# Kernel tuning notes

Hardware: AMD Instinct MI355X
Metric: run time of the kernel (lower is better)

The kernel has to match this reference:

```python
import jax, jax.numpy as jnp
import numpy as np

N = 50000
E = 800000
IN_DIM = 128
H1 = 512
H2 = 300
OUT_DIM = 10
EPS = 1e-5


def setup_inputs() -> dict:
    key = jax.random.key(0)
    ks = jax.random.split(key, 12)
    x = jax.random.normal(ks[0], (N, IN_DIM), dtype=jnp.float32)
    edge_index = jax.random.randint(ks[1], (2, E), 0, N, dtype=jnp.int64)
    edge_weight = jax.random.uniform(ks[2], (E,), dtype=jnp.float32)
    def glorot(k, fan_in, fan_out):
        lim = np.sqrt(6.0 / (fan_in + fan_out)).astype(np.float32)
        return jax.random.uniform(k, (fan_in, fan_out), jnp.float32, -lim, lim)
    return {
        "x": x,
        "edge_index": edge_index,
        "edge_weight": edge_weight,
        "W1": glorot(ks[3], IN_DIM, H1), "b1": jnp.zeros((H1,), jnp.float32),
        "g1": jnp.ones((H1,), jnp.float32), "beta1": jnp.zeros((H1,), jnp.float32),
        "W2": glorot(ks[4], H1, H2), "b2": jnp.zeros((H2,), jnp.float32),
        "g2": jnp.ones((H2,), jnp.float32), "beta2": jnp.zeros((H2,), jnp.float32),
        "Wl": glorot(ks[5], H2, OUT_DIM), "bl": jnp.zeros((OUT_DIM,), jnp.float32),
    }


def _gcn_norm(edge_index, edge_weight, n):
    # add self loops (fill value 1.0), then symmetric normalization (PyG gcn_norm)
    si = jnp.arange(n, dtype=edge_index.dtype)
    row = jnp.concatenate([edge_index[0], si])  # source
    col = jnp.concatenate([edge_index[1], si])  # target
    w = jnp.concatenate([edge_weight, jnp.ones((n,), edge_weight.dtype)])
    deg = jax.ops.segment_sum(w, col, num_segments=n)
    dis = jnp.where(deg > 0, jax.lax.rsqrt(deg), 0.0)
    return row, col, dis[row] * w * dis[col]


def _propagate(h, row, col, norm, n):
    # gather source rows, weight, scatter-add into targets
    return jax.ops.segment_sum(h[row] * norm[:, None], col, num_segments=n)


def _batchnorm(h, g, beta):
    mean = jnp.mean(h, axis=0)
    var = jnp.mean(jnp.square(h - mean), axis=0)  # biased var (torch BN)
    return (h - mean) * jax.lax.rsqrt(var + EPS) * g + beta


def reference(x, edge_index, edge_weight, W1, b1, g1, beta1,
              W2, b2, g2, beta2, Wl, bl):
    n = x.shape[0]
    row, col, norm = _gcn_norm(edge_index, edge_weight, n)
    # layer 1: aggregate then transform (== GCNConv's lin-then-propagate math)
    h = _propagate(x, row, col, norm, n) @ W1 + b1
    h = jax.nn.relu(_batchnorm(h, g1, beta1))
    # layer 2: transform then aggregate
    h = _propagate(h @ W2, row, col, norm, n) + b2
    h = jax.nn.relu(_batchnorm(h, g2, beta2))
    # classifier head + log_softmax
    h = jax.nn.relu(h @ Wl + bl)
    return jax.nn.log_softmax(h, axis=1)
```

## Files before the change

### kernel.cpp

```cpp
#include <hip/hip_runtime.h>
#include <math.h>

namespace {

constexpr int kIn  = 128;
constexpr int kH1  = 512;
constexpr int kH2  = 300;
constexpr int kH2p = 304;
constexpr int kW2R = 384;
constexpr int kOut = 10;
constexpr float kEps = 1e-5f;

typedef __attribute__((ext_vector_type(8))) short bf16x8;
typedef __attribute__((ext_vector_type(4))) float f32x4;

__device__ __forceinline__ void atomAddF(float* p, float v) { unsafeAtomicAdd(p, v); }

__device__ __forceinline__ unsigned short f2bf(float f) {
  unsigned u = __builtin_bit_cast(unsigned, f);
  unsigned r = u + 0x7fffu + ((u >> 16) & 1u);
  return (unsigned short)(r >> 16);
}
__device__ __forceinline__ float bf2f(unsigned short h) {
  return __builtin_bit_cast(float, (unsigned)h << 16);
}
__device__ __forceinline__ float blo(unsigned u) { return __builtin_bit_cast(float, u << 16); }
__device__ __forceinline__ float bhi(unsigned u) { return __builtin_bit_cast(float, u & 0xffff0000u); }
__device__ __forceinline__ unsigned pk2(float a, float b) {
  return (unsigned)f2bf(a) | ((unsigned)f2bf(b) << 16);
}

__device__ __forceinline__ void gload16(const unsigned short* g, unsigned short* l) {
  __builtin_amdgcn_global_load_lds(
      (const __attribute__((address_space(1))) unsigned int*)g,
      (__attribute__((address_space(3))) unsigned int*)l, 16, 0, 0);
}

__device__ __forceinline__ void fma8(const uint4& q, float w, float* acc) {
  acc[0] = fmaf(blo(q.x), w, acc[0]);
  acc[1] = fmaf(bhi(q.x), w, acc[1]);
  acc[2] = fmaf(blo(q.y), w, acc[2]);
  acc[3] = fmaf(bhi(q.y), w, acc[3]);
  acc[4] = fmaf(blo(q.z), w, acc[4]);
  acc[5] = fmaf(bhi(q.z), w, acc[5]);
  acc[6] = fmaf(blo(q.w), w, acc[6]);
  acc[7] = fmaf(bhi(q.w), w, acc[7]);
}

__global__ void k_prep(float* __restrict__ deg, int* __restrict__ cnt,
                       const float* __restrict__ x, unsigned short* __restrict__ xbf,
                       float* __restrict__ st,
                       const float* __restrict__ W1, unsigned short* __restrict__ W1T,
                       const float* __restrict__ W2, unsigned short* __restrict__ W2T, int n) {
  int i = blockIdx.x * blockDim.x + threadIdx.x;
  if (i < n) { deg[i] = 1.0f; cnt[i] = 0; }
  if (i < 4096) st[i] = 0.f;
  if (i < kIn * kH1) {
    int nn = i / kIn, k = i - nn * kIn;
    W1T[i] = f2bf(W1[(size_t)k * kH1 + nn]);
  }
  if (i < kW2R * kH1) {
    int nn = i / kH1, k = i - nn * kH1;
    W2T[i] = (nn < kH2) ? f2bf(W2[(size_t)k * kH2 + nn]) : (unsigned short)0;
  }
  if (i < n * 16) {
    int node = i >> 4, g = i & 15;
    const float4* xp = reinterpret_cast<const float4*>(x + (size_t)node * kIn + g * 8);
    float4 v0 = xp[0], v1 = xp[1];
    uint4 o;
    o.x = pk2(v0.x, v0.y); o.y = pk2(v0.z, v0.w);
    o.z = pk2(v1.x, v1.y); o.w = pk2(v1.z, v1.w);
    reinterpret_cast<uint4*>(xbf)[i] = o;
  }
}

__global__ void k_deg_cnt(float* __restrict__ deg, int* __restrict__ cnt,
                          const int* __restrict__ ei, const float* __restrict__ w, int nE) {
  int i = blockIdx.x * blockDim.x + threadIdx.x;
  if (i < nE) {
    int c = ei[nE + i];
    atomAddF(&deg[c], w[i]);
    atomicAdd(&cnt[c], 1);
  }
}

__global__ void k_dis(float* __restrict__ deg, int n) {
  int i = blockIdx.x * blockDim.x + threadIdx.x;
  if (i < n) deg[i] = rsqrtf(deg[i]);
}

__global__ __launch_bounds__(1024) void k_scan(int* __restrict__ cnt, int n) {
  __shared__ int wsum[16];
  __shared__ int woff[17];
  const int lane = threadIdx.x & 63;
  const int wid  = threadIdx.x >> 6;
  int carry = 0;
  const int nchunk = (n + 1023) >> 10;
  for (int ch = 0; ch < nchunk; ++ch) {
    int i = (ch << 10) + threadIdx.x;
    int v = (i < n) ? cnt[i] : 0;
    int s = v;
#pragma unroll
    for (int off = 1; off < 64; off <<= 1) {
      int t = __shfl_up(s, off);
      if (lane >= off) s += t;
    }
    if (lane == 63) wsum[wid] = s;
    __syncthreads();
    if (wid == 0 && lane < 16) {
      int u = wsum[lane];
#pragma unroll
      for (int off = 1; off < 16; off <<= 1) {
        int q = __shfl_up(u, off);
        if (lane >= off) u += q;
      }
      woff[lane + 1] = u;
      if (lane == 0) woff[0] = 0;
    }
    __syncthreads();
    int excl = s - v + woff[wid] + carry;
    if (i < n) cnt[i] = excl;
    carry += woff[16];
    __syncthreads();
  }
}

__global__ void k_scatter(int* __restrict__ cnt, const int* __restrict__ ei,
                          const float* __restrict__ w, const float* __restrict__ dis,
                          uint2* __restrict__ pr, int nE) {
  int i = blockIdx.x * blockDim.x + threadIdx.x;
  if (i < nE) {
    int r = ei[i];
    int c = ei[nE + i];
    int pos = atomicAdd(&cnt[c], 1);
    float ww = dis[r] * w[i] * dis[c];
    pr[pos] = make_uint2((unsigned)r, __builtin_bit_cast(unsigned, ww));
  }
}

template<int NSQ>
__global__ void k_gather(const unsigned short* __restrict__ X, const int* __restrict__ endp,
                         const uint2* __restrict__ pr, const float* __restrict__ dis,
                         unsigned short* __restrict__ out, int n) {
  int tid = blockIdx.x * blockDim.x + threadIdx.x;
  int v = tid / NSQ;
  int s = tid - v * NSQ;
  if (v >= n) return;
  int beg = (v == 0) ? 0 : endp[v - 1];
  int end = endp[v];
  const uint4* Xr = reinterpret_cast<const uint4*>(X);
  float d = dis[v];
  float sw = d * d;
  float acc[8];
  {
    uint4 q = Xr[(size_t)v * NSQ + s];
    acc[0] = blo(q.x) * sw; acc[1] = bhi(q.x) * sw;
    acc[2] = blo(q.y) * sw; acc[3] = bhi(q.y) * sw;
    acc[4] = blo(q.z) * sw; acc[5] = bhi(q.z) * sw;
    acc[6] = blo(q.w) * sw; acc[7] = bhi(q.w) * sw;
  }
  int e = beg;
  for (; e + 4 <= end; e += 4) {
    uint2 p0 = pr[e], p1 = pr[e + 1], p2 = pr[e + 2], p3 = pr[e + 3];
    uint4 q0 = Xr[(size_t)p0.x * NSQ + s];
    uint4 q1 = Xr[(size_t)p1.x * NSQ + s];
    uint4 q2 = Xr[(size_t)p2.x * NSQ + s];
    uint4 q3 = Xr[(size_t)p3.x * NSQ + s];
    fma8(q0, __builtin_bit_cast(float, p0.y), acc);
    fma8(q1, __builtin_bit_cast(float, p1.y), acc);
    fma8(q2, __builtin_bit_cast(float, p2.y), acc);
    fma8(q3, __builtin_bit_cast(float, p3.y), acc);
  }
  for (; e < end; ++e) {
    uint2 p = pr[e];
    uint4 q = Xr[(size_t)p.x * NSQ + s];
    fma8(q, __builtin_bit_cast(float, p.y), acc);
  }
  uint4 o;
  o.x = pk2(acc[0], acc[1]);
  o.y = pk2(acc[2], acc[3]);
  o.z = pk2(acc[4], acc[5]);
  o.w = pk2(acc[6], acc[7]);
  reinterpret_cast<uint4*>(out)[(size_t)v * NSQ + s] = o;
}

__global__ __launch_bounds__(256) void k_gemm(const unsigned short* __restrict__ A,
    const unsigned short* __restrict__ BT, unsigned short* __restrict__ C,
    int M, int Nlog, int K, int ntiles, int nwg) {
  constexpr int BK = 64;
  __shared__ unsigned short lA[(BK / 8) * 128 * 8];
  __shared__ unsigned short lB[(BK / 8) * 128 * 8];

  int p = blockIdx.x;
  int xcd = p & 7, idx = p >> 3;
  int q8 = nwg >> 3, r8 = nwg & 7;
  int logical = (xcd < r8 ? xcd * (q8 + 1) : r8 * (q8 + 1) + (xcd - r8) * q8) + idx;
  const int nt = logical % ntiles;
  const int mt = logical / ntiles;
  const int m0 = mt * 128, n0 = nt * 128;

  const int tid = threadIdx.x, lane = tid & 63, wid = tid >> 6;
  const int wr = wid >> 1, wc = wid & 1;
  const int fr = lane & 15, fq = lane >> 4;

  int arow[4], brow[4], k8s[4];
#pragma unroll
  for (int j = 0; j < 4; ++j) {
    int g = tid + 256 * j;
    int row = g & 127;
    k8s[j] = g >> 7;
    int ar = m0 + row;
    arow[j] = (ar < M) ? ar : (M - 1);
    brow[j] = n0 + row;
  }

  f32x4 acc[4][4] = {};

  for (int k0 = 0; k0 < K; k0 += BK) {
    __syncthreads();
#pragma unroll
    for (int j = 0; j < 4; ++j) {
      int g = tid + 256 * j;
      gload16(A  + (size_t)arow[j] * K + k0 + k8s[j] * 8, &lA[g * 8]);
      gload16(BT + (size_t)brow[j] * K + k0 + k8s[j] * 8, &lB[g * 8]);
    }
    __syncthreads();
#pragma unroll
    for (int step = 0; step < 2; ++step) {
      bf16x8 af[4], bf[4];
#pragma unroll
      for (int m = 0; m < 4; ++m)
        af[m] = *reinterpret_cast<const bf16x8*>(
            &lA[(((step * 4 + fq) << 7) + wr * 64 + m * 16 + fr) * 8]);
#pragma unroll
      for (int nn = 0; nn < 4; ++nn)
        bf[nn] = *reinterpret_cast<const bf16x8*>(
            &lB[(((step * 4 + fq) << 7) + wc * 64 + nn * 16 + fr) * 8]);
#pragma unroll
      for (int m = 0; m < 4; ++m)
#pragma unroll
        for (int nn = 0; nn < 4; ++nn)
          acc[m][nn] = __builtin_amdgcn_mfma_f32_16x16x32_bf16(af[m], bf[nn], acc[m][nn], 0, 0, 0);
    }
  }

#pragma unroll
  for (int m = 0; m < 4; ++m) {
#pragma unroll
    for (int r = 0; r < 4; ++r) {
      int row = m0 + wr * 64 + m * 16 + fq * 4 + r;
      if (row >= M) continue;
#pragma unroll
      for (int nn = 0; nn < 4; ++nn) {
        int col = n0 + wc * 64 + nn * 16 + fr;
        if (col < Nlog)
          C[(size_t)row * Nlog + col] = f2bf(acc[m][nn][r]);
      }
    }
  }
}

__global__ void k_bn_stats_bf16(const unsigned short* __restrict__ H, float* __restrict__ s1,
                                float* __restrict__ s2, int n, int C, int stride, int rpb) {
  int r0 = blockIdx.x * rpb;
  int r1 = r0 + rpb;
  if (r1 > n) r1 = n;
  for (int c = threadIdx.x; c < C; c += blockDim.x) {
    float a = 0.f, b = 0.f;
    for (int r = r0; r < r1; ++r) {
      float v = bf2f(H[(size_t)r * stride + c]);
      a += v;
      b = fmaf(v, v, b);
    }
    atomAddF(&s1[c], a);
    atomAddF(&s2[c], b);
  }
}

__global__ void k_bn_finalize(const float* __restrict__ s1, const float* __restrict__ s2,
                              const float* __restrict__ g, const float* __restrict__ beta,
                              float* __restrict__ scale, float* __restrict__ shift,
                              int C, float invN) {
  int c = blockIdx.x * blockDim.x + threadIdx.x;
  if (c >= C) return;
  float mean = s1[c] * invN;
  float var = fmaxf(s2[c] * invN - mean * mean, 0.f);
  float sc = g[c] * rsqrtf(var + kEps);
  scale[c] = sc;
  shift[c] = beta[c] - mean * sc;
}

template<int C>
__global__ void k_bn_apply_relu_bf16(unsigned short* __restrict__ H,
                                     const float* __restrict__ scale,
                                     const float* __restrict__ shift, int total8) {
  int i = blockIdx.x * blockDim.x + threadIdx.x;
  if (i >= total8) return;
  uint4 q = reinterpret_cast<uint4*>(H)[i];
  int c = (i * 8) & (C - 1);
  unsigned w[4] = {q.x, q.y, q.z, q.w};
  unsigned o[4];
#pragma unroll
  for (int j = 0; j < 4; ++j) {
    float lo = blo(w[j]);
    float hi = bhi(w[j]);
    int cl = c + j * 2;
    lo = fmaxf(fmaf(lo, scale[cl],     shift[cl]),     0.f);
    hi = fmaxf(fmaf(hi, scale[cl + 1], shift[cl + 1]), 0.f);
    o[j] = pk2(lo, hi);
  }
  reinterpret_cast<uint4*>(H)[i] = make_uint4(o[0], o[1], o[2], o[3]);
}

__global__ __launch_bounds__(256) void k_head(const unsigned short* __restrict__ H,
    const float* __restrict__ scale, const float* __restrict__ shift,
    const float* __restrict__ Wl, const float* __restrict__ bl,
    float* __restrict__ out, int n) {
  __shared__ float sW[kH2 * kOut];
  __shared__ float sScale[kH2], sShift[kH2];
  for (int i = threadIdx.x; i < kH2 * kOut; i += blockDim.x) sW[i] = Wl[i];
  for (int i = threadIdx.x; i < kH2; i += blockDim.x) {
    sScale[i] = scale[i];
    sShift[i] = shift[i];
  }
  __syncthreads();
  float blv[kOut];
#pragma unroll
  for (int j = 0; j < kOut; ++j) blv[j] = bl[j];
  const int lane = threadIdx.x & 63;
  const int wid = (blockIdx.x * blockDim.x + threadIdx.x) >> 6;
  const int nw  = (gridDim.x * blockDim.x) >> 6;
  for (int node = wid; node < n; node += nw) {
    const unsigned short* hrow = H + (size_t)node * kH2p;
    float acc[kOut] = {};
    for (int k = lane; k < kH2; k += 64) {
      float v = fmaxf(fmaf(bf2f(hrow[k]), sScale[k], sShift[k]), 0.f);
      const float* wr = sW + k * kOut;
#pragma unroll
      for (int j = 0; j < kOut; ++j) acc[j] = fmaf(v, wr[j], acc[j]);
    }
#pragma unroll
    for (int j = 0; j < kOut; ++j) {
      float v = acc[j];
      for (int off = 32; off > 0; off >>= 1) v += __shfl_down(v, off);
      acc[j] = v;
    }
    if (lane == 0) {
      float vv[kOut], m = -1e30f;
#pragma unroll
      for (int j = 0; j < kOut; ++j) {
        vv[j] = fmaxf(acc[j] + blv[j], 0.f);
        m = fmaxf(m, vv[j]);
      }
      float s = 0.f;
#pragma unroll
      for (int j = 0; j < kOut; ++j) s += expf(vv[j] - m);
      float lse = m + logf(s);
      float* o = out + (size_t)node * kOut;
#pragma unroll
      for (int j = 0; j < kOut; ++j) o[j] = vv[j] - lse;
    }
  }
}

}

extern "C" void kernel_launch(void* const* d_in, const int* in_sizes, int n_in,
                              void* d_out, int out_size, void* d_ws, size_t ws_size,
                              hipStream_t stream) {
  const float* x   = (const float*)d_in[0];
  const int*   ei  = (const int*)d_in[1];
  const float* ew  = (const float*)d_in[2];
  const float* W1  = (const float*)d_in[3];
  const float* g1  = (const float*)d_in[5];
  const float* be1 = (const float*)d_in[6];
  const float* W2  = (const float*)d_in[7];
  const float* g2  = (const float*)d_in[9];
  const float* be2 = (const float*)d_in[10];
  const float* Wl  = (const float*)d_in[11];
  const float* bl  = (const float*)d_in[12];
  float* out = (float*)d_out;
  float* ws  = (float*)d_ws;

  const int n = in_sizes[0] / kIn;
  const int e = in_sizes[1] / 2;

  float* dis = ws;
  int*   cnt = (int*)(ws + 50048);
  uint2* pr  = (uint2*)(ws + 100096);
  float* st  = ws + 1700096;
  float* s1a = st,        *s2a = st + 512,  *sc1 = st + 1024, *sh1 = st + 1536;
  float* s1b = st + 2048, *s2b = st + 2560, *sc2 = st + 3072, *sh2 = st + 3584;
  unsigned short* xbf = (unsigned short*)(ws + 1704192);
  unsigned short* W1T = (unsigned short*)(ws + 4904192);
  unsigned short* W2T = (unsigned short*)(ws + 4936960);
  unsigned short* agg1 = (unsigned short*)(ws + 5035264);
  unsigned short* h1   = (unsigned short*)(ws + 8235264);
  unsigned short* t2   = (unsigned short*)(ws + 21035264);
  unsigned short* agg2 = (unsigned short*)(ws + 28635264);

  constexpr int TPB = 256;

  k_prep<<<(n * 16 + TPB - 1) / TPB, TPB, 0, stream>>>(dis, cnt, x, xbf, st, W1, W1T, W2, W2T, n);
  k_deg_cnt<<<(e + TPB - 1) / TPB, TPB, 0, stream>>>(dis, cnt, ei, ew, e);
  k_dis<<<(n + TPB - 1) / TPB, TPB, 0, stream>>>(dis, n);
  k_scan<<<1, 1024, 0, stream>>>(cnt, n);
  k_scatter<<<(e + TPB - 1) / TPB, TPB, 0, stream>>>(cnt, ei, ew, dis, pr, e);

  const int mtiles = (n + 127) / 128;

  {
    int tot = n * (kIn / 8);
    k_gather<kIn / 8><<<(tot + TPB - 1) / TPB, TPB, 0, stream>>>(xbf, cnt, pr, dis, agg1, n);
  }
  {
    int ntiles = kH1 / 128;
    int nwg = mtiles * ntiles;
    k_gemm<<<nwg, 256, 0, stream>>>(agg1, W1T, h1, n, kH1, kIn, ntiles, nwg);
  }
  k_bn_stats_bf16<<<512, 256, 0, stream>>>(h1, s1a, s2a, n, kH1, kH1, (n + 511) / 512);
  k_bn_finalize<<<(kH1 + 255) / 256, 256, 0, stream>>>(s1a, s2a, g1, be1, sc1, sh1, kH1, 1.0f / n);
  k_bn_apply_relu_bf16<kH1><<<((n * (kH1 / 8)) + TPB - 1) / TPB, TPB, 0, stream>>>(
      h1, sc1, sh1, n * (kH1 / 8));

  {
    int ntiles = kW2R / 128;
    int nwg = mtiles * ntiles;
    k_gemm<<<nwg, 256, 0, stream>>>(h1, W2T, t2, n, kH2p, kH1, ntiles, nwg);
  }
  {
    int tot = n * (kH2p / 8);
    k_gather<kH2p / 8><<<(tot + TPB - 1) / TPB, TPB, 0, stream>>>(t2, cnt, pr, dis, agg2, n);
  }
  k_bn_stats_bf16<<<512, 256, 0, stream>>>(agg2, s1b, s2b, n, kH2, kH2p, (n + 511) / 512);
  k_bn_finalize<<<(kH2 + 255) / 256, 256, 0, stream>>>(s1b, s2b, g2, be2, sc2, sh2, kH2, 1.0f / n);

  k_head<<<1024, 256, 0, stream>>>(agg2, sc2, sh2, Wl, bl, out, n);
}
```

Baseline: 556.2 us.

## Slice gather feature matrices into 8 column slabs and parallelize CSR scan

The gather-source feature matrices (bf16 x and the layer-2 GEMM output) are stored as 8 column-sliced slabs, each contiguous over nodes. The gather kernel assigns block index mod 8 to a slice, so each slice's random-row working set is smaller and more likely to stay cache-resident, and it writes back in row-major order. The gather loop is unrolled to 8 edges with nontemporal loads of the edge list and nontemporal stores of the output, and layer-2 padding grows from 304 to 320 columns. The single-block serial scan becomes a three-kernel block-parallel scan, which adds two extra launches.

After: 685.5 us. 1.23x slower.

```diff
diff --git a/kernel.cpp b/kernel.cpp
--- a/kernel.cpp
+++ b/kernel.cpp
@@ -6,13 +6,14 @@
 constexpr int kIn  = 128;
 constexpr int kH1  = 512;
 constexpr int kH2  = 300;
-constexpr int kH2p = 304;
+constexpr int kH2s = 320;
 constexpr int kW2R = 384;
 constexpr int kOut = 10;
 constexpr float kEps = 1e-5f;
 
 typedef __attribute__((ext_vector_type(8))) short bf16x8;
 typedef __attribute__((ext_vector_type(4))) float f32x4;
+typedef __attribute__((ext_vector_type(4))) unsigned int u32x4;
 
 __device__ __forceinline__ void atomAddF(float* p, float v) { unsafeAtomicAdd(p, v); }
 
@@ -70,7 +71,8 @@
     uint4 o;
     o.x = pk2(v0.x, v0.y); o.y = pk2(v0.z, v0.w);
     o.z = pk2(v1.x, v1.y); o.w = pk2(v1.z, v1.w);
-    reinterpret_cast<uint4*>(xbf)[i] = o;
+    int slice = g >> 1, win = g & 1;
+    reinterpret_cast<uint4*>(xbf)[((size_t)slice * n + node) * 2 + win] = o;
   }
 }
 
@@ -89,40 +91,50 @@
   if (i < n) deg[i] = rsqrtf(deg[i]);
 }
 
-__global__ __launch_bounds__(1024) void k_scan(int* __restrict__ cnt, int n) {
-  __shared__ int wsum[16];
-  __shared__ int woff[17];
-  const int lane = threadIdx.x & 63;
-  const int wid  = threadIdx.x >> 6;
-  int carry = 0;
-  const int nchunk = (n + 1023) >> 10;
-  for (int ch = 0; ch < nchunk; ++ch) {
-    int i = (ch << 10) + threadIdx.x;
-    int v = (i < n) ? cnt[i] : 0;
-    int s = v;
-#pragma unroll
-    for (int off = 1; off < 64; off <<= 1) {
-      int t = __shfl_up(s, off);
-      if (lane >= off) s += t;
-    }
-    if (lane == 63) wsum[wid] = s;
-    __syncthreads();
-    if (wid == 0 && lane < 16) {
-      int u = wsum[lane];
-#pragma unroll
-      for (int off = 1; off < 16; off <<= 1) {
-        int q = __shfl_up(u, off);
-        if (lane >= off) u += q;
-      }
-      woff[lane + 1] = u;
-      if (lane == 0) woff[0] = 0;
-    }
-    __syncthreads();
-    int excl = s - v + woff[wid] + carry;
-    if (i < n) cnt[i] = excl;
-    carry += woff[16];
-    __syncthreads();
-  }
+__global__ void k_scan_a(int* __restrict__ cnt, int* __restrict__ bsum, int n) {
+  __shared__ int ws[4];
+  int i = blockIdx.x * 256 + threadIdx.x;
+  int lane = threadIdx.x & 63, wid = threadIdx.x >> 6;
+  int v = (i < n) ? cnt[i] : 0;
+  int s = v;
+#pragma unroll
+  for (int off = 1; off < 64; off <<= 1) {
+    int t = __shfl_up(s, off);
+    if (lane >= off) s += t;
+  }
+  if (lane == 63) ws[wid] = s;
+  __syncthreads();
+  int add = 0;
+  if (wid > 0) add += ws[0];
+  if (wid > 1) add += ws[1];
+  if (wid > 2) add += ws[2];
+  if (i < n) cnt[i] = s - v + add;
+  if (threadIdx.x == 255) bsum[blockIdx.x] = add + s;
+}
+
+__global__ void k_scan_b(int* __restrict__ bsum, int nb) {
+  __shared__ int ws[4];
+  int i = threadIdx.x;
+  int lane = i & 63, wid = i >> 6;
+  int v = (i < nb) ? bsum[i] : 0;
+  int s = v;
+#pragma unroll
+  for (int off = 1; off < 64; off <<= 1) {
+    int t = __shfl_up(s, off);
+    if (lane >= off) s += t;
+  }
+  if (lane == 63) ws[wid] = s;
+  __syncthreads();
+  int add = 0;
+  if (wid > 0) add += ws[0];
+  if (wid > 1) add += ws[1];
+  if (wid > 2) add += ws[2];
+  if (i < nb) bsum[i] = s - v + add;
+}
+
+__global__ void k_scan_c(int* __restrict__ cnt, const int* __restrict__ bsum, int n) {
+  int i = blockIdx.x * 256 + threadIdx.x;
+  if (i < n) cnt[i] += bsum[blockIdx.x];
 }
 
 __global__ void k_scatter(int* __restrict__ cnt, const int* __restrict__ ei,
@@ -142,13 +154,14 @@
 __global__ void k_gather(const unsigned short* __restrict__ X, const int* __restrict__ endp,
                          const uint2* __restrict__ pr, const float* __restrict__ dis,
                          unsigned short* __restrict__ out, int n) {
-  int tid = blockIdx.x * blockDim.x + threadIdx.x;
+  const int slice = blockIdx.x & 7;
+  int tid = (blockIdx.x >> 3) * blockDim.x + threadIdx.x;
   int v = tid / NSQ;
   int s = tid - v * NSQ;
   if (v >= n) return;
+  const uint4* Xr = reinterpret_cast<const uint4*>(X) + (size_t)slice * n * NSQ;
   int beg = (v == 0) ? 0 : endp[v - 1];
   int end = endp[v];
-  const uint4* Xr = reinterpret_cast<const uint4*>(X);
   float d = dis[v];
   float sw = d * d;
   float acc[8];
@@ -159,31 +172,34 @@
     acc[4] = blo(q.z) * sw; acc[5] = bhi(q.z) * sw;
     acc[6] = blo(q.w) * sw; acc[7] = bhi(q.w) * sw;
   }
+  const unsigned long long* pru = reinterpret_cast<const unsigned long long*>(pr);
   int e = beg;
-  for (; e + 4 <= end; e += 4) {
-    uint2 p0 = pr[e], p1 = pr[e + 1], p2 = pr[e + 2], p3 = pr[e + 3];
-    uint4 q0 = Xr[(size_t)p0.x * NSQ + s];
-    uint4 q1 = Xr[(size_t)p1.x * NSQ + s];
-    uint4 q2 = Xr[(size_t)p2.x * NSQ + s];
-    uint4 q3 = Xr[(size_t)p3.x * NSQ + s];
-    fma8(q0, __builtin_bit_cast(float, p0.y), acc);
-    fma8(q1, __builtin_bit_cast(float, p1.y), acc);
-    fma8(q2, __builtin_bit_cast(float, p2.y), acc);
-    fma8(q3, __builtin_bit_cast(float, p3.y), acc);
+  for (; e + 8 <= end; e += 8) {
+    unsigned long long p[8];
+    uint4 q[8];
+#pragma unroll
+    for (int j = 0; j < 8; ++j) p[j] = __builtin_nontemporal_load(pru + e + j);
+#pragma unroll
+    for (int j = 0; j < 8; ++j) q[j] = Xr[(size_t)(unsigned)p[j] * NSQ + s];
+#pragma unroll
+    for (int j = 0; j < 8; ++j)
+      fma8(q[j], __builtin_bit_cast(float, (unsigned)(p[j] >> 32)), acc);
   }
   for (; e < end; ++e) {
-    uint2 p = pr[e];
-    uint4 q = Xr[(size_t)p.x * NSQ + s];
-    fma8(q, __builtin_bit_cast(float, p.y), acc);
-  }
-  uint4 o;
-  o.x = pk2(acc[0], acc[1]);
-  o.y = pk2(acc[2], acc[3]);
-  o.z = pk2(acc[4], acc[5]);
-  o.w = pk2(acc[6], acc[7]);
-  reinterpret_cast<uint4*>(out)[(size_t)v * NSQ + s] = o;
-}
-
+    unsigned long long pj = __builtin_nontemporal_load(pru + e);
+    uint4 q = Xr[(size_t)(unsigned)pj * NSQ + s];
+    fma8(q, __builtin_bit_cast(float, (unsigned)(pj >> 32)), acc);
+  }
+  u32x4 o;
+  o[0] = pk2(acc[0], acc[1]);
+  o[1] = pk2(acc[2], acc[3]);
+  o[2] = pk2(acc[4], acc[5]);
+  o[3] = pk2(acc[6], acc[7]);
+  __builtin_nontemporal_store(
+      o, reinterpret_cast<u32x4*>(out) + (size_t)v * (8 * NSQ) + slice * NSQ + s);
+}
+
+template<bool SLICED_OUT>
 __global__ __launch_bounds__(256) void k_gemm(const unsigned short* __restrict__ A,
     const unsigned short* __restrict__ BT, unsigned short* __restrict__ C,
     int M, int Nlog, int K, int ntiles, int nwg) {
@@ -253,8 +269,15 @@
 #pragma unroll
       for (int nn = 0; nn < 4; ++nn) {
         int col = n0 + wc * 64 + nn * 16 + fr;
-        if (col < Nlog)
-          C[(size_t)row * Nlog + col] = f2bf(acc[m][nn][r]);
+        if (col < Nlog) {
+          unsigned short vv = f2bf(acc[m][nn][r]);
+          if constexpr (SLICED_OUT) {
+            int slice = col / 40, cw = col - slice * 40;
+            C[((size_t)slice * M + row) * 40 + cw] = vv;
+          } else {
+            C[(size_t)row * Nlog + col] = vv;
+          }
+        }
       }
     }
   }
@@ -331,7 +354,7 @@
   const int wid = (blockIdx.x * blockDim.x + threadIdx.x) >> 6;
   const int nw  = (gridDim.x * blockDim.x) >> 6;
   for (int node = wid; node < n; node += nw) {
-    const unsigned short* hrow = H + (size_t)node * kH2p;
+    const unsigned short* hrow = H + (size_t)node * kH2s;
     float acc[kOut] = {};
     for (int k = lane; k < kH2; k += 64) {
       float v = fmaxf(fmaf(bf2f(hrow[k]), sScale[k], sShift[k]), 0.f);
@@ -391,32 +414,36 @@
   float* st  = ws + 1700096;
   float* s1a = st,        *s2a = st + 512,  *sc1 = st + 1024, *sh1 = st + 1536;
   float* s1b = st + 2048, *s2b = st + 2560, *sc2 = st + 3072, *sh2 = st + 3584;
-  unsigned short* xbf = (unsigned short*)(ws + 1704192);
-  unsigned short* W1T = (unsigned short*)(ws + 4904192);
-  unsigned short* W2T = (unsigned short*)(ws + 4936960);
-  unsigned short* agg1 = (unsigned short*)(ws + 5035264);
-  unsigned short* h1   = (unsigned short*)(ws + 8235264);
-  unsigned short* t2   = (unsigned short*)(ws + 21035264);
-  unsigned short* agg2 = (unsigned short*)(ws + 28635264);
+  int*   bsum = (int*)(ws + 1704192);
+  unsigned short* xbf = (unsigned short*)(ws + 1704704);
+  unsigned short* W1T = (unsigned short*)(ws + 4904704);
+  unsigned short* W2T = (unsigned short*)(ws + 4937472);
+  unsigned short* agg1 = (unsigned short*)(ws + 5035776);
+  unsigned short* h1   = (unsigned short*)(ws + 8235776);
+  unsigned short* t2   = (unsigned short*)(ws + 21035776);
+  unsigned short* agg2 = (unsigned short*)(ws + 29035776);
 
   constexpr int TPB = 256;
+  const int nb = (n + 255) / 256;
 
   k_prep<<<(n * 16 + TPB - 1) / TPB, TPB, 0, stream>>>(dis, cnt, x, xbf, st, W1, W1T, W2, W2T, n);
   k_deg_cnt<<<(e + TPB - 1) / TPB, TPB, 0, stream>>>(dis, cnt, ei, ew, e);
   k_dis<<<(n + TPB - 1) / TPB, TPB, 0, stream>>>(dis, n);
-  k_scan<<<1, 1024, 0, stream>>>(cnt, n);
+  k_scan_a<<<nb, 256, 0, stream>>>(cnt, bsum, n);
+  k_scan_b<<<1, 256, 0, stream>>>(bsum, nb);
+  k_scan_c<<<nb, 256, 0, stream>>>(cnt, bsum, n);
   k_scatter<<<(e + TPB - 1) / TPB, TPB, 0, stream>>>(cnt, ei, ew, dis, pr, e);
 
   const int mtiles = (n + 127) / 128;
 
   {
-    int tot = n * (kIn / 8);
-    k_gather<kIn / 8><<<(tot + TPB - 1) / TPB, TPB, 0, stream>>>(xbf, cnt, pr, dis, agg1, n);
+    int bps = (n * 2 + TPB - 1) / TPB;
+    k_gather<2><<<bps * 8, TPB, 0, stream>>>(xbf, cnt, pr, dis, agg1, n);
   }
   {
     int ntiles = kH1 / 128;
     int nwg = mtiles * ntiles;
-    k_gemm<<<nwg, 256, 0, stream>>>(agg1, W1T, h1, n, kH1, kIn, ntiles, nwg);
+    k_gemm<false><<<nwg, 256, 0, stream>>>(agg1, W1T, h1, n, kH1, kIn, ntiles, nwg);
   }
   k_bn_stats_bf16<<<512, 256, 0, stream>>>(h1, s1a, s2a, n, kH1, kH1, (n + 511) / 512);
   k_bn_finalize<<<(kH1 + 255) / 256, 256, 0, stream>>>(s1a, s2a, g1, be1, sc1, sh1, kH1, 1.0f / n);
@@ -426,13 +453,13 @@
   {
     int ntiles = kW2R / 128;
     int nwg = mtiles * ntiles;
-    k_gemm<<<nwg, 256, 0, stream>>>(h1, W2T, t2, n, kH2p, kH1, ntiles, nwg);
+    k_gemm<true><<<nwg, 256, 0, stream>>>(h1, W2T, t2, n, kH2s, kH1, ntiles, nwg);
   }
   {
-    int tot = n * (kH2p / 8);
-    k_gather<kH2p / 8><<<(tot + TPB - 1) / TPB, TPB, 0, stream>>>(t2, cnt, pr, dis, agg2, n);
-  }
-  k_bn_stats_bf16<<<512, 256, 0, stream>>>(agg2, s1b, s2b, n, kH2, kH2p, (n + 511) / 512);
+    int bps = (n * 5 + TPB - 1) / TPB;
+    k_gather<5><<<bps * 8, TPB, 0, stream>>>(t2, cnt, pr, dis, agg2, n);
+  }
+  k_bn_stats_bf16<<<512, 256, 0, stream>>>(agg2, s1b, s2b, n, kH2, kH2s, (n + 511) / 512);
   k_bn_finalize<<<(kH2 + 255) / 256, 256, 0, stream>>>(s1b, s2b, g2, be2, sc2, sh2, kH2, 1.0f / n);
 
   k_head<<<1024, 256, 0, stream>>>(agg2, sc2, sh2, Wl, bl, out, n);
```

## Parallelize prefix scan across blocks and vectorize batchnorm statistics reduction

Applied to the files above, without the earlier changes.

Replaces the single-workgroup serial-chunk exclusive scan over node counts with a three-pass multi-block scan (block scan, scan of block sums, add-back). Rewrites the batchnorm statistics kernel so each thread loads 8 bf16 channels at once with 128-bit loads, splits rows across 4 wavefronts, and reduces in shared memory before the atomics. Both target latency-bound serial work in small kernels, at the cost of two extra launches for the scan. The stats kernel assumes C/8 ≤ 64 channel groups and uses padded stride 304 for layer 2, where padded columns are presumed harmless.

Result: faster. 534.9 us (-3.8%).

```diff
diff --git a/kernel.cpp b/kernel.cpp
--- a/kernel.cpp
+++ b/kernel.cpp
@@ -89,40 +89,50 @@
   if (i < n) deg[i] = rsqrtf(deg[i]);
 }
 
-__global__ __launch_bounds__(1024) void k_scan(int* __restrict__ cnt, int n) {
-  __shared__ int wsum[16];
-  __shared__ int woff[17];
-  const int lane = threadIdx.x & 63;
-  const int wid  = threadIdx.x >> 6;
-  int carry = 0;
-  const int nchunk = (n + 1023) >> 10;
-  for (int ch = 0; ch < nchunk; ++ch) {
-    int i = (ch << 10) + threadIdx.x;
-    int v = (i < n) ? cnt[i] : 0;
-    int s = v;
-#pragma unroll
-    for (int off = 1; off < 64; off <<= 1) {
-      int t = __shfl_up(s, off);
-      if (lane >= off) s += t;
-    }
-    if (lane == 63) wsum[wid] = s;
-    __syncthreads();
-    if (wid == 0 && lane < 16) {
-      int u = wsum[lane];
-#pragma unroll
-      for (int off = 1; off < 16; off <<= 1) {
-        int q = __shfl_up(u, off);
-        if (lane >= off) u += q;
-      }
-      woff[lane + 1] = u;
-      if (lane == 0) woff[0] = 0;
-    }
-    __syncthreads();
-    int excl = s - v + woff[wid] + carry;
-    if (i < n) cnt[i] = excl;
-    carry += woff[16];
-    __syncthreads();
-  }
+__global__ void k_scan_a(int* __restrict__ cnt, int* __restrict__ bsum, int n) {
+  __shared__ int ws[4];
+  int i = blockIdx.x * 256 + threadIdx.x;
+  int lane = threadIdx.x & 63, wid = threadIdx.x >> 6;
+  int v = (i < n) ? cnt[i] : 0;
+  int s = v;
+#pragma unroll
+  for (int off = 1; off < 64; off <<= 1) {
+    int t = __shfl_up(s, off);
+    if (lane >= off) s += t;
+  }
+  if (lane == 63) ws[wid] = s;
+  __syncthreads();
+  int add = 0;
+  if (wid > 0) add += ws[0];
+  if (wid > 1) add += ws[1];
+  if (wid > 2) add += ws[2];
+  if (i < n) cnt[i] = s - v + add;
+  if (threadIdx.x == 255) bsum[blockIdx.x] = add + s;
+}
+
+__global__ void k_scan_b(int* __restrict__ bsum, int nb) {
+  __shared__ int ws[4];
+  int i = threadIdx.x;
+  int lane = i & 63, wid = i >> 6;
+  int v = (i < nb) ? bsum[i] : 0;
+  int s = v;
+#pragma unroll
+  for (int off = 1; off < 64; off <<= 1) {
+    int t = __shfl_up(s, off);
+    if (lane >= off) s += t;
+  }
+  if (lane == 63) ws[wid] = s;
+  __syncthreads();
+  int add = 0;
+  if (wid > 0) add += ws[0];
+  if (wid > 1) add += ws[1];
+  if (wid > 2) add += ws[2];
+  if (i < nb) bsum[i] = s - v + add;
+}
+
+__global__ void k_scan_c(int* __restrict__ cnt, const int* __restrict__ bsum, int n) {
+  int i = blockIdx.x * 256 + threadIdx.x;
+  if (i < n) cnt[i] += bsum[blockIdx.x];
 }
 
 __global__ void k_scatter(int* __restrict__ cnt, const int* __restrict__ ei,
@@ -260,20 +270,46 @@
   }
 }
 
-__global__ void k_bn_stats_bf16(const unsigned short* __restrict__ H, float* __restrict__ s1,
-                                float* __restrict__ s2, int n, int C, int stride, int rpb) {
+template<int C>
+__global__ __launch_bounds__(256) void k_bn_stats_co(const unsigned short* __restrict__ H,
+                                                     float* __restrict__ s1, float* __restrict__ s2,
+                                                     int n, int rpb) {
+  constexpr int G = C / 8;
+  __shared__ float redS[3][G][8];
+  __shared__ float redQ[3][G][8];
+  const int g = threadIdx.x & 63;
+  const int rr = threadIdx.x >> 6;
   int r0 = blockIdx.x * rpb;
-  int r1 = r0 + rpb;
-  if (r1 > n) r1 = n;
-  for (int c = threadIdx.x; c < C; c += blockDim.x) {
-    float a = 0.f, b = 0.f;
-    for (int r = r0; r < r1; ++r) {
-      float v = bf2f(H[(size_t)r * stride + c]);
-      a += v;
-      b = fmaf(v, v, b);
-    }
-    atomAddF(&s1[c], a);
-    atomAddF(&s2[c], b);
+  int r1 = r0 + rpb; if (r1 > n) r1 = n;
+  float sa[8] = {}, sq[8] = {};
+  if (g < G) {
+    for (int r = r0 + rr; r < r1; r += 4) {
+      uint4 q = *reinterpret_cast<const uint4*>(H + (size_t)r * C + g * 8);
+      float v[8] = {blo(q.x), bhi(q.x), blo(q.y), bhi(q.y),
+                    blo(q.z), bhi(q.z), blo(q.w), bhi(q.w)};
+#pragma unroll
+      for (int j = 0; j < 8; ++j) {
+        sa[j] += v[j];
+        sq[j] = fmaf(v[j], v[j], sq[j]);
+      }
+    }
+    if (rr > 0) {
+#pragma unroll
+      for (int j = 0; j < 8; ++j) {
+        redS[rr - 1][g][j] = sa[j];
+        redQ[rr - 1][g][j] = sq[j];
+      }
+    }
+  }
+  __syncthreads();
+  if (rr == 0 && g < G) {
+#pragma unroll
+    for (int j = 0; j < 8; ++j) {
+      float ts = sa[j] + redS[0][g][j] + redS[1][g][j] + redS[2][g][j];
+      float tq = sq[j] + redQ[0][g][j] + redQ[1][g][j] + redQ[2][g][j];
+      atomAddF(&s1[g * 8 + j], ts);
+      atomAddF(&s2[g * 8 + j], tq);
+    }
   }
 }
 
@@ -391,20 +427,25 @@
   float* st  = ws + 1700096;
   float* s1a = st,        *s2a = st + 512,  *sc1 = st + 1024, *sh1 = st + 1536;
   float* s1b = st + 2048, *s2b = st + 2560, *sc2 = st + 3072, *sh2 = st + 3584;
-  unsigned short* xbf = (unsigned short*)(ws + 1704192);
-  unsigned short* W1T = (unsigned short*)(ws + 4904192);
-  unsigned short* W2T = (unsigned short*)(ws + 4936960);
-  unsigned short* agg1 = (unsigned short*)(ws + 5035264);
-  unsigned short* h1   = (unsigned short*)(ws + 8235264);
-  unsigned short* t2   = (unsigned short*)(ws + 21035264);
-  unsigned short* agg2 = (unsigned short*)(ws + 28635264);
+  int*   bsum = (int*)(ws + 1704192);
+  unsigned short* xbf = (unsigned short*)(ws + 1704704);
+  unsigned short* W1T = (unsigned short*)(ws + 4904704);
+  unsigned short* W2T = (unsigned short*)(ws + 4937472);
+  unsigned short* agg1 = (unsigned short*)(ws + 5035776);
+  unsigned short* h1   = (unsigned short*)(ws + 8235776);
+  unsigned short* t2   = (unsigned short*)(ws + 21035776);
+  unsigned short* agg2 = (unsigned short*)(ws + 28635776);
 
   constexpr int TPB = 256;
+  const int nb = (n + 255) / 256;
+  const int rpb = (n + 255) / 256;
 
   k_prep<<<(n * 16 + TPB - 1) / TPB, TPB, 0, stream>>>(dis, cnt, x, xbf, st, W1, W1T, W2, W2T, n);
   k_deg_cnt<<<(e + TPB - 1) / TPB, TPB, 0, stream>>>(dis, cnt, ei, ew, e);
   k_dis<<<(n + TPB - 1) / TPB, TPB, 0, stream>>>(dis, n);
-  k_scan<<<1, 1024, 0, stream>>>(cnt, n);
+  k_scan_a<<<nb, 256, 0, stream>>>(cnt, bsum, n);
+  k_scan_b<<<1, 256, 0, stream>>>(bsum, nb);
+  k_scan_c<<<nb, 256, 0, stream>>>(cnt, bsum, n);
   k_scatter<<<(e + TPB - 1) / TPB, TPB, 0, stream>>>(cnt, ei, ew, dis, pr, e);
 
   const int mtiles = (n + 127) / 128;
@@ -418,7 +459,7 @@
     int nwg = mtiles * ntiles;
     k_gemm<<<nwg, 256, 0, stream>>>(agg1, W1T, h1, n, kH1, kIn, ntiles, nwg);
   }
-  k_bn_stats_bf16<<<512, 256, 0, stream>>>(h1, s1a, s2a, n, kH1, kH1, (n + 511) / 512);
+  k_bn_stats_co<kH1><<<256, 256, 0, stream>>>(h1, s1a, s2a, n, rpb);
   k_bn_finalize<<<(kH1 + 255) / 256, 256, 0, stream>>>(s1a, s2a, g1, be1, sc1, sh1, kH1, 1.0f / n);
   k_bn_apply_relu_bf16<kH1><<<((n * (kH1 / 8)) + TPB - 1) / TPB, TPB, 0, stream>>>(
       h1, sc1, sh1, n * (kH1 / 8));
@@ -432,7 +473,7 @@
     int tot = n * (kH2p / 8);
     k_gather<kH2p / 8><<<(tot + TPB - 1) / TPB, TPB, 0, stream>>>(t2, cnt, pr, dis, agg2, n);
   }
-  k_bn_stats_bf16<<<512, 256, 0, stream>>>(agg2, s1b, s2b, n, kH2, kH2p, (n + 511) / 512);
+  k_bn_stats_co<kH2p><<<256, 256, 0, stream>>>(agg2, s1b, s2b, n, rpb);
   k_bn_finalize<<<(kH2 + 255) / 256, 256, 0, stream>>>(s1b, s2b, g2, be2, sc2, sh2, kH2, 1.0f / n);
 
   k_head<<<1024, 256, 0, stream>>>(agg2, sc2, sh2, Wl, bl, out, n);
```
